# Performance work log

Measured on AMD Instinct MI355X. Metric: run time of the kernel, lower is better.

The kernel has to match this reference:

```python
import jax, jax.numpy as jnp
import numpy as np

E, K = 8, 2
B, S, H = 8, 2048, 512
R0, R1, O = 256, 256, 512
T = B * S


def _make_routing(key):
    # Mixtral-style: top-k softmax weights [T, K] and one-hot mask [E, K, T]
    k1, k2 = jax.random.split(key)
    sel = jax.random.randint(k1, (T, K), 0, E)                      # selected expert per (token, slot)
    rw = jax.nn.softmax(jax.random.normal(k2, (T, K)), axis=-1)
    mask = jax.nn.one_hot(sel, E, dtype=jnp.bool_)                  # [T, K, E]
    mask = jnp.transpose(mask, (2, 1, 0))                           # [E, K, T]
    return mask, rw


def setup_inputs() -> dict:
    key = jax.random.key(0)
    ks = jax.random.split(key, 10)
    x = jax.random.normal(ks[0], (B, S, H), dtype=jnp.float32)
    m1, rw1 = _make_routing(ks[1])
    m2, rw2 = _make_routing(ks[2])
    m3, rw3 = _make_routing(ks[3])
    s = 0.02
    W1 = jax.random.normal(ks[4], (E, R0, H), dtype=jnp.float32) * s
    b1 = jnp.zeros((E, R0), dtype=jnp.float32)
    W2 = jax.random.normal(ks[5], (E, R1, R0), dtype=jnp.float32) * s
    b2 = jnp.zeros((E, R1), dtype=jnp.float32)
    W3 = jax.random.normal(ks[6], (E, O, R1), dtype=jnp.float32) * s
    b3 = jnp.zeros((E, O), dtype=jnp.float32)
    return {"x": x,
            "expert_mask1": m1, "expert_mask2": m2, "expert_mask3": m3,
            "routing_weights1": rw1, "routing_weights2": rw2, "routing_weights3": rw3,
            "W1": W1, "b1": b1, "W2": W2, "b2": b2, "W3": W3, "b3": b3}


def _moe_stage(h, mask, rw, W, b, act):
    # combine[e, t] = routing weight of token t for expert e (0 if not routed)
    cmb = jnp.einsum('ekt,tk->et', mask.astype(h.dtype), rw)
    acc0 = jnp.zeros((h.shape[0], W.shape[1]), dtype=h.dtype)

    def body(acc, ew):
        Wi, bi, ci = ew            # Wi: [out, in], bi: [out], ci: [T]
        out = h @ Wi.T + bi
        if act:
            out = jax.nn.relu(out)
        return acc + ci[:, None] * out, None

    acc, _ = jax.lax.scan(body, acc0, (W, b, cmb))
    return acc


def reference(x, expert_mask1, expert_mask2, expert_mask3,
              routing_weights1, routing_weights2, routing_weights3,
              W1, b1, W2, b2, W3, b3):
    bsz, seq, dim = x.shape
    h = x.reshape(-1, dim)                                          # [T, H]
    h = _moe_stage(h, expert_mask1, routing_weights1, W1, b1, act=False)   # [T, R0]
    h = _moe_stage(h, expert_mask2, routing_weights2, W2, b2, act=False)   # [T, R1]
    h = _moe_stage(h, expert_mask3, routing_weights3, W3, b3, act=True)    # relu on expert output, then combine
    out = jax.nn.relu(h.reshape(bsz, seq, -1))
    return out
```

## Files before the change

### kernel.cpp

```cpp
#include <hip/hip_runtime.h>

#define T_TOKENS 16384
#define CAP 12288
#define CNT_STRIDE 16

typedef unsigned short u16;
typedef __attribute__((ext_vector_type(8))) short short8;
typedef __attribute__((ext_vector_type(4))) float float4v;

__device__ __forceinline__ u16 f2b(float f) {
  unsigned u = __float_as_uint(f);
  u = (u + 0x7fffu + ((u >> 16) & 1u)) >> 16;
  return (u16)u;
}
__device__ __forceinline__ float b2f(u16 h) {
  return __uint_as_float(((unsigned)h) << 16);
}

__global__ void convert_w(const float* __restrict__ W1, const float* __restrict__ W2,
                          const float* __restrict__ W3, u16* __restrict__ Wb1,
                          u16* __restrict__ Wb2, u16* __restrict__ Wb3) {
  const int n1 = 8 * 256 * 512, n2 = 8 * 256 * 256;
  int base = (blockIdx.x * 256 + threadIdx.x) * 8;
  const float* src;
  u16* dst;
  int off = base;
  if (base < n1) { src = W1; dst = Wb1; }
  else if (base < n1 + n2) { src = W2; dst = Wb2; off = base - n1; }
  else { src = W3; dst = Wb3; off = base - n1 - n2; }
  float4 a0 = *(const float4*)(src + off);
  float4 a1 = *(const float4*)(src + off + 4);
  short8 v;
  v[0] = (short)f2b(a0.x); v[1] = (short)f2b(a0.y);
  v[2] = (short)f2b(a0.z); v[3] = (short)f2b(a0.w);
  v[4] = (short)f2b(a1.x); v[5] = (short)f2b(a1.y);
  v[6] = (short)f2b(a1.z); v[7] = (short)f2b(a1.w);
  *(short8*)(dst + off) = v;
}

__global__ void route_kernel(const int* __restrict__ m1, const int* __restrict__ m2,
                             const int* __restrict__ m3, const float* __restrict__ rw1,
                             const float* __restrict__ rw2, const float* __restrict__ rw3,
                             int* __restrict__ cnt, int* __restrict__ idxbuf,
                             float* __restrict__ wgtbuf) {
  __shared__ int lcnt[24];
  __shared__ int lbase[24];
  const int tid = threadIdx.x;
  const int t = blockIdx.x * 256 + tid;
  if (tid < 24) lcnt[tid] = 0;
  __syncthreads();

  const int* masks[3] = {m1, m2, m3};
  const float* rws[3] = {rw1, rw2, rw3};
  int expert[3][2], lpos[3][2];
#pragma unroll
  for (int s = 0; s < 3; ++s)
#pragma unroll
    for (int k = 0; k < 2; ++k) {
      int e = 0;
#pragma unroll
      for (int j = 0; j < 8; ++j)
        if (masks[s][(j * 2 + k) * T_TOKENS + t] != 0) e = j;
      expert[s][k] = e;
      lpos[s][k] = atomicAdd(&lcnt[s * 8 + e], 1);
    }
  __syncthreads();
  if (tid < 24) lbase[tid] = atomicAdd(&cnt[tid * CNT_STRIDE], lcnt[tid]);
  __syncthreads();
#pragma unroll
  for (int s = 0; s < 3; ++s)
#pragma unroll
    for (int k = 0; k < 2; ++k) {
      int e = expert[s][k];
      int p = lbase[s * 8 + e] + lpos[s][k];
      if (p < CAP) {
        idxbuf[(s * 8 + e) * CAP + p] = t * 2 + k;
        wgtbuf[(s * 8 + e) * CAP + p] = rws[s][t * 2 + k];
      }
    }
}

template <int KDIM, int NDIM_TOTAL, int SRC, int RELU>
__global__ __launch_bounds__(256) void moe_gemm(
    const void* __restrict__ Asrc, const u16* __restrict__ Wb, const float* __restrict__ bias,
    const int* __restrict__ cnt, const int* __restrict__ idxbuf, const float* __restrict__ wgtbuf,
    u16* __restrict__ outTmp) {
  __shared__ __align__(16) u16 As[64][72];
  __shared__ __align__(16) u16 Bs[256][72];
  __shared__ int rowTok[64];
  __shared__ float rowW[64];

  const int e = blockIdx.y;
  const int n_e = cnt[e * CNT_STRIDE];
  const int row0 = blockIdx.x * 64;
  if (row0 >= n_e) return;
  const int nbase = blockIdx.z * 256;
  const int tid = threadIdx.x;

  if (tid < 64) {
    int g = row0 + tid;
    if (g < n_e) {
      rowTok[tid] = idxbuf[e * CAP + g];
      rowW[tid] = wgtbuf[e * CAP + g];
    } else {
      rowTok[tid] = 0;
      rowW[tid] = 0.f;
    }
  }
  __syncthreads();

  const int wave = tid >> 6, lane = tid & 63;
  const int lrow = lane & 15, lquad = lane >> 4;
  const int arow = tid >> 3;
  const int acol = (tid & 7) * 8;

  float4v acc[4][4];
#pragma unroll
  for (int i = 0; i < 4; ++i)
#pragma unroll
    for (int j = 0; j < 4; ++j) acc[i][j] = (float4v)0.f;

  const u16* Wbe = Wb + ((size_t)e * NDIM_TOTAL + nbase) * KDIM;

  for (int kb = 0; kb < KDIM; kb += 64) {
#pragma unroll
    for (int it = 0; it < 2; ++it) {
      int r = arow + it * 32;
      int tok = rowTok[r];
      short8 v;
      if (SRC == 0) {
        const float* xp = (const float*)Asrc + (size_t)(tok >> 1) * KDIM + kb + acol;
        float4 a0 = *(const float4*)xp;
        float4 a1 = *(const float4*)(xp + 4);
        v[0] = (short)f2b(a0.x); v[1] = (short)f2b(a0.y);
        v[2] = (short)f2b(a0.z); v[3] = (short)f2b(a0.w);
        v[4] = (short)f2b(a1.x); v[5] = (short)f2b(a1.y);
        v[6] = (short)f2b(a1.z); v[7] = (short)f2b(a1.w);
      } else {
        const u16* p0 = (const u16*)Asrc + ((size_t)(tok >> 1) * 2) * KDIM + kb + acol;
        short8 v0 = *(const short8*)p0;
        short8 v1 = *(const short8*)(p0 + KDIM);
#pragma unroll
        for (int j = 0; j < 8; ++j)
          v[j] = (short)f2b(b2f((u16)v0[j]) + b2f((u16)v1[j]));
      }
      *(short8*)&As[r][acol] = v;
    }
#pragma unroll
    for (int it = 0; it < 8; ++it) {
      int r = arow + it * 32;
      *(short8*)&Bs[r][acol] = *(const short8*)(Wbe + (size_t)r * KDIM + kb + acol);
    }
    __syncthreads();
#pragma unroll
    for (int ks = 0; ks < 64; ks += 32) {
      short8 af[4], bfr[4];
#pragma unroll
      for (int mt = 0; mt < 4; ++mt)
        af[mt] = *(const short8*)&As[mt * 16 + lrow][ks + lquad * 8];
#pragma unroll
      for (int nt = 0; nt < 4; ++nt)
        bfr[nt] = *(const short8*)&Bs[wave * 64 + nt * 16 + lrow][ks + lquad * 8];
#pragma unroll
      for (int mt = 0; mt < 4; ++mt)
#pragma unroll
        for (int nt = 0; nt < 4; ++nt)
          acc[mt][nt] = __builtin_amdgcn_mfma_f32_16x16x32_bf16(af[mt], bfr[nt], acc[mt][nt], 0, 0, 0);
    }
    __syncthreads();
  }

  float bv[4];
#pragma unroll
  for (int nt = 0; nt < 4; ++nt)
    bv[nt] = bias[e * NDIM_TOTAL + nbase + wave * 64 + nt * 16 + lrow];
#pragma unroll
  for (int mt = 0; mt < 4; ++mt) {
#pragma unroll
    for (int i = 0; i < 4; ++i) {
      int m = mt * 16 + lquad * 4 + i;
      if (row0 + m < n_e) {
        float w = rowW[m];
        size_t drow = (size_t)rowTok[m] * NDIM_TOTAL + nbase;
#pragma unroll
        for (int nt = 0; nt < 4; ++nt) {
          float v = acc[mt][nt][i] + bv[nt];
          if (RELU) v = fmaxf(v, 0.f);
          v *= w;
          outTmp[drow + wave * 64 + nt * 16 + lrow] = f2b(v);
        }
      }
    }
  }
}

__global__ void finalize_kernel(const u16* __restrict__ tmp3, float* __restrict__ out) {
  int f = (blockIdx.x * 256 + threadIdx.x) * 8;
  int t = f >> 9;
  int o = f & 511;
  const u16* p = tmp3 + (size_t)t * 1024 + o;
  short8 v0 = *(const short8*)p;
  short8 v1 = *(const short8*)(p + 512);
  float4 r0, r1;
  r0.x = fmaxf(b2f((u16)v0[0]) + b2f((u16)v1[0]), 0.f);
  r0.y = fmaxf(b2f((u16)v0[1]) + b2f((u16)v1[1]), 0.f);
  r0.z = fmaxf(b2f((u16)v0[2]) + b2f((u16)v1[2]), 0.f);
  r0.w = fmaxf(b2f((u16)v0[3]) + b2f((u16)v1[3]), 0.f);
  r1.x = fmaxf(b2f((u16)v0[4]) + b2f((u16)v1[4]), 0.f);
  r1.y = fmaxf(b2f((u16)v0[5]) + b2f((u16)v1[5]), 0.f);
  r1.z = fmaxf(b2f((u16)v0[6]) + b2f((u16)v1[6]), 0.f);
  r1.w = fmaxf(b2f((u16)v0[7]) + b2f((u16)v1[7]), 0.f);
  *(float4*)(out + f) = r0;
  *(float4*)(out + f + 4) = r1;
}

extern "C" void kernel_launch(void* const* d_in, const int* in_sizes, int n_in,
                              void* d_out, int out_size, void* d_ws, size_t ws_size,
                              hipStream_t stream) {
  const float* x  = (const float*)d_in[0];
  const int* m1   = (const int*)d_in[1];
  const int* m2   = (const int*)d_in[2];
  const int* m3   = (const int*)d_in[3];
  const float* rw1 = (const float*)d_in[4];
  const float* rw2 = (const float*)d_in[5];
  const float* rw3 = (const float*)d_in[6];
  const float* W1 = (const float*)d_in[7];
  const float* b1 = (const float*)d_in[8];
  const float* W2 = (const float*)d_in[9];
  const float* b2 = (const float*)d_in[10];
  const float* W3 = (const float*)d_in[11];
  const float* b3 = (const float*)d_in[12];
  float* out = (float*)d_out;

  char* ws = (char*)d_ws;
  size_t off = 0;
  int* cnt = (int*)(ws + off); off += 24 * CNT_STRIDE * 4;
  u16* Wb1 = (u16*)(ws + off); off += (size_t)8 * 256 * 512 * 2;
  u16* Wb2 = (u16*)(ws + off); off += (size_t)8 * 256 * 256 * 2;
  u16* Wb3 = (u16*)(ws + off); off += (size_t)8 * 512 * 256 * 2;
  u16* tmp1 = (u16*)(ws + off); off += (size_t)T_TOKENS * 2 * 256 * 2;
  u16* tmp2 = (u16*)(ws + off); off += (size_t)T_TOKENS * 2 * 256 * 2;
  u16* tmp3 = (u16*)(ws + off); off += (size_t)T_TOKENS * 2 * 512 * 2;
  int* idxb = (int*)(ws + off); off += (size_t)3 * 8 * CAP * 4;
  float* wgtb = (float*)(ws + off); off += (size_t)3 * 8 * CAP * 4;

  hipMemsetAsync(cnt, 0, 24 * CNT_STRIDE * 4, stream);
  convert_w<<<1280, 256, 0, stream>>>(W1, W2, W3, Wb1, Wb2, Wb3);
  route_kernel<<<64, 256, 0, stream>>>(m1, m2, m3, rw1, rw2, rw3, cnt, idxb, wgtb);

  moe_gemm<512, 256, 0, 0><<<dim3(CAP / 64, 8, 1), 256, 0, stream>>>(
      x, Wb1, b1, cnt + 0, idxb + 0, wgtb + 0, tmp1);
  moe_gemm<256, 256, 1, 0><<<dim3(CAP / 64, 8, 1), 256, 0, stream>>>(
      tmp1, Wb2, b2, cnt + 8 * CNT_STRIDE, idxb + 8 * CAP, wgtb + 8 * CAP, tmp2);
  moe_gemm<256, 512, 1, 1><<<dim3(CAP / 64, 8, 2), 256, 0, stream>>>(
      tmp2, Wb3, b3, cnt + 16 * CNT_STRIDE, idxb + 16 * CAP, wgtb + 16 * CAP, tmp3);

  finalize_kernel<<<4096, 256, 0, stream>>>(tmp3, out);
}
```

Before: 194.6 us.

## Use direct global-to-LDS loads with XOR swizzle and precombine activations

The GEMM operand staging now uses global_load_lds (16-byte direct-to-LDS transfers) into an unpadded, XOR-swizzled shared layout instead of register round-trips. To make that possible, x is converted to bf16 up front and separate combine kernels sum the two top-k slot outputs into dense bf16 activations before the next stage. This removes the per-tile conversion and summation from the GEMM inner loop and cuts VGPR traffic. In exchange it adds two extra kernels and extra HBM writes and reads of the intermediate buffers.

```diff
diff --git a/kernel.cpp b/kernel.cpp
--- a/kernel.cpp
+++ b/kernel.cpp
@@ -5,8 +5,12 @@
 #define CNT_STRIDE 16
 
 typedef unsigned short u16;
+typedef unsigned int u32;
 typedef __attribute__((ext_vector_type(8))) short short8;
 typedef __attribute__((ext_vector_type(4))) float float4v;
+
+typedef __attribute__((address_space(1))) u32 gas_u32;
+typedef __attribute__((address_space(3))) u32 las_u32;
 
 __device__ __forceinline__ u16 f2b(float f) {
   unsigned u = __float_as_uint(f);
@@ -16,18 +20,23 @@
 __device__ __forceinline__ float b2f(u16 h) {
   return __uint_as_float(((unsigned)h) << 16);
 }
-
-__global__ void convert_w(const float* __restrict__ W1, const float* __restrict__ W2,
-                          const float* __restrict__ W3, u16* __restrict__ Wb1,
-                          u16* __restrict__ Wb2, u16* __restrict__ Wb3) {
-  const int n1 = 8 * 256 * 512, n2 = 8 * 256 * 256;
+__device__ __forceinline__ void gload16(const u16* g, u16* l) {
+  __builtin_amdgcn_global_load_lds((gas_u32*)g, (las_u32*)l, 16, 0, 0);
+}
+
+__global__ void convert_all(const float* __restrict__ W1, const float* __restrict__ W2,
+                            const float* __restrict__ W3, const float* __restrict__ x,
+                            u16* __restrict__ Wb1, u16* __restrict__ Wb2,
+                            u16* __restrict__ Wb3, u16* __restrict__ xb) {
+  const int n1 = 8 * 256 * 512, n2 = 8 * 256 * 256, n3 = 8 * 512 * 256;
   int base = (blockIdx.x * 256 + threadIdx.x) * 8;
   const float* src;
   u16* dst;
   int off = base;
   if (base < n1) { src = W1; dst = Wb1; }
   else if (base < n1 + n2) { src = W2; dst = Wb2; off = base - n1; }
-  else { src = W3; dst = Wb3; off = base - n1 - n2; }
+  else if (base < n1 + n2 + n3) { src = W3; dst = Wb3; off = base - n1 - n2; }
+  else { src = x; dst = xb; off = base - n1 - n2 - n3; }
   float4 a0 = *(const float4*)(src + off);
   float4 a1 = *(const float4*)(src + off + 4);
   short8 v;
@@ -80,13 +89,13 @@
     }
 }
 
-template <int KDIM, int NDIM_TOTAL, int SRC, int RELU>
+template <int KDIM, int NDIM_TOTAL, int RELU>
 __global__ __launch_bounds__(256) void moe_gemm(
-    const void* __restrict__ Asrc, const u16* __restrict__ Wb, const float* __restrict__ bias,
+    const u16* __restrict__ Asrc, const u16* __restrict__ Wb, const float* __restrict__ bias,
     const int* __restrict__ cnt, const int* __restrict__ idxbuf, const float* __restrict__ wgtbuf,
     u16* __restrict__ outTmp) {
-  __shared__ __align__(16) u16 As[64][72];
-  __shared__ __align__(16) u16 Bs[256][72];
+  __shared__ __align__(16) u16 As[64 * 64];
+  __shared__ __align__(16) u16 Bs[256 * 64];
   __shared__ int rowTok[64];
   __shared__ float rowW[64];
 
@@ -111,8 +120,15 @@
 
   const int wave = tid >> 6, lane = tid & 63;
   const int lrow = lane & 15, lquad = lane >> 4;
-  const int arow = tid >> 3;
-  const int acol = (tid & 7) * 8;
+  const int srow = lane >> 3;
+  const int gsw = (lane & 7) ^ srow;
+
+  const u16* aP0 = Asrc + (size_t)(rowTok[(wave * 2 + 0) * 8 + srow] >> 1) * KDIM + gsw * 8;
+  const u16* aP1 = Asrc + (size_t)(rowTok[(wave * 2 + 1) * 8 + srow] >> 1) * KDIM + gsw * 8;
+  const u16* Wbe = Wb + ((size_t)e * NDIM_TOTAL + nbase) * KDIM;
+  const u16* bP = Wbe + (size_t)(wave * 64 + srow) * KDIM + gsw * 8;
+  u16* aD = As + (wave * 2) * 512;
+  u16* bD = Bs + (wave * 8) * 512;
 
   float4v acc[4][4];
 #pragma unroll
@@ -120,47 +136,23 @@
 #pragma unroll
     for (int j = 0; j < 4; ++j) acc[i][j] = (float4v)0.f;
 
-  const u16* Wbe = Wb + ((size_t)e * NDIM_TOTAL + nbase) * KDIM;
-
   for (int kb = 0; kb < KDIM; kb += 64) {
-#pragma unroll
-    for (int it = 0; it < 2; ++it) {
-      int r = arow + it * 32;
-      int tok = rowTok[r];
-      short8 v;
-      if (SRC == 0) {
-        const float* xp = (const float*)Asrc + (size_t)(tok >> 1) * KDIM + kb + acol;
-        float4 a0 = *(const float4*)xp;
-        float4 a1 = *(const float4*)(xp + 4);
-        v[0] = (short)f2b(a0.x); v[1] = (short)f2b(a0.y);
-        v[2] = (short)f2b(a0.z); v[3] = (short)f2b(a0.w);
-        v[4] = (short)f2b(a1.x); v[5] = (short)f2b(a1.y);
-        v[6] = (short)f2b(a1.z); v[7] = (short)f2b(a1.w);
-      } else {
-        const u16* p0 = (const u16*)Asrc + ((size_t)(tok >> 1) * 2) * KDIM + kb + acol;
-        short8 v0 = *(const short8*)p0;
-        short8 v1 = *(const short8*)(p0 + KDIM);
-#pragma unroll
-        for (int j = 0; j < 8; ++j)
-          v[j] = (short)f2b(b2f((u16)v0[j]) + b2f((u16)v1[j]));
-      }
-      *(short8*)&As[r][acol] = v;
-    }
-#pragma unroll
-    for (int it = 0; it < 8; ++it) {
-      int r = arow + it * 32;
-      *(short8*)&Bs[r][acol] = *(const short8*)(Wbe + (size_t)r * KDIM + kb + acol);
-    }
+    gload16(aP0 + kb, aD);
+    gload16(aP1 + kb, aD + 512);
+#pragma unroll
+    for (int i = 0; i < 8; ++i)
+      gload16(bP + (size_t)i * 8 * KDIM + kb, bD + i * 512);
     __syncthreads();
 #pragma unroll
     for (int ks = 0; ks < 64; ks += 32) {
+      const int gq = ((ks >> 3) + lquad) ^ (lrow & 7);
       short8 af[4], bfr[4];
 #pragma unroll
       for (int mt = 0; mt < 4; ++mt)
-        af[mt] = *(const short8*)&As[mt * 16 + lrow][ks + lquad * 8];
+        af[mt] = *(const short8*)&As[(mt * 16 + lrow) * 64 + gq * 8];
 #pragma unroll
       for (int nt = 0; nt < 4; ++nt)
-        bfr[nt] = *(const short8*)&Bs[wave * 64 + nt * 16 + lrow][ks + lquad * 8];
+        bfr[nt] = *(const short8*)&Bs[(wave * 64 + nt * 16 + lrow) * 64 + gq * 8];
 #pragma unroll
       for (int mt = 0; mt < 4; ++mt)
 #pragma unroll
@@ -192,6 +184,21 @@
       }
     }
   }
+}
+
+template <int NDIM>
+__global__ void combine_kernel(const u16* __restrict__ tmp, u16* __restrict__ h) {
+  int base = (blockIdx.x * 256 + threadIdx.x) * 8;
+  int t = base / NDIM;
+  int o = base % NDIM;
+  const u16* p = tmp + ((size_t)t * 2) * NDIM + o;
+  short8 v0 = *(const short8*)p;
+  short8 v1 = *(const short8*)(p + NDIM);
+  short8 r;
+#pragma unroll
+  for (int j = 0; j < 8; ++j)
+    r[j] = (short)f2b(b2f((u16)v0[j]) + b2f((u16)v1[j]));
+  *(short8*)(h + base) = r;
 }
 
 __global__ void finalize_kernel(const u16* __restrict__ tmp3, float* __restrict__ out) {
@@ -238,22 +245,27 @@
   u16* Wb1 = (u16*)(ws + off); off += (size_t)8 * 256 * 512 * 2;
   u16* Wb2 = (u16*)(ws + off); off += (size_t)8 * 256 * 256 * 2;
   u16* Wb3 = (u16*)(ws + off); off += (size_t)8 * 512 * 256 * 2;
+  u16* xb  = (u16*)(ws + off); off += (size_t)T_TOKENS * 512 * 2;
   u16* tmp1 = (u16*)(ws + off); off += (size_t)T_TOKENS * 2 * 256 * 2;
+  u16* h1  = (u16*)(ws + off); off += (size_t)T_TOKENS * 256 * 2;
   u16* tmp2 = (u16*)(ws + off); off += (size_t)T_TOKENS * 2 * 256 * 2;
+  u16* h2  = (u16*)(ws + off); off += (size_t)T_TOKENS * 256 * 2;
   u16* tmp3 = (u16*)(ws + off); off += (size_t)T_TOKENS * 2 * 512 * 2;
   int* idxb = (int*)(ws + off); off += (size_t)3 * 8 * CAP * 4;
   float* wgtb = (float*)(ws + off); off += (size_t)3 * 8 * CAP * 4;
 
   hipMemsetAsync(cnt, 0, 24 * CNT_STRIDE * 4, stream);
-  convert_w<<<1280, 256, 0, stream>>>(W1, W2, W3, Wb1, Wb2, Wb3);
+  convert_all<<<5376, 256, 0, stream>>>(W1, W2, W3, x, Wb1, Wb2, Wb3, xb);
   route_kernel<<<64, 256, 0, stream>>>(m1, m2, m3, rw1, rw2, rw3, cnt, idxb, wgtb);
 
-  moe_gemm<512, 256, 0, 0><<<dim3(CAP / 64, 8, 1), 256, 0, stream>>>(
-      x, Wb1, b1, cnt + 0, idxb + 0, wgtb + 0, tmp1);
-  moe_gemm<256, 256, 1, 0><<<dim3(CAP / 64, 8, 1), 256, 0, stream>>>(
-      tmp1, Wb2, b2, cnt + 8 * CNT_STRIDE, idxb + 8 * CAP, wgtb + 8 * CAP, tmp2);
-  moe_gemm<256, 512, 1, 1><<<dim3(CAP / 64, 8, 2), 256, 0, stream>>>(
-      tmp2, Wb3, b3, cnt + 16 * CNT_STRIDE, idxb + 16 * CAP, wgtb + 16 * CAP, tmp3);
+  moe_gemm<512, 256, 0><<<dim3(CAP / 64, 8, 1), 256, 0, stream>>>(
+      xb, Wb1, b1, cnt + 0, idxb + 0, wgtb + 0, tmp1);
+  combine_kernel<256><<<2048, 256, 0, stream>>>(tmp1, h1);
+  moe_gemm<256, 256, 0><<<dim3(CAP / 64, 8, 1), 256, 0, stream>>>(
+      h1, Wb2, b2, cnt + 8 * CNT_STRIDE, idxb + 8 * CAP, wgtb + 8 * CAP, tmp2);
+  combine_kernel<256><<<2048, 256, 0, stream>>>(tmp2, h2);
+  moe_gemm<256, 512, 1><<<dim3(CAP / 64, 8, 2), 256, 0, stream>>>(
+      h2, Wb3, b3, cnt + 16 * CNT_STRIDE, idxb + 16 * CAP, wgtb + 16 * CAP, tmp3);
 
   finalize_kernel<<<4096, 256, 0, stream>>>(tmp3, out);
 }
```

Measured after the change: 191.6 us. Within noise of the previous version (-1.5%).

## Load weight tiles directly into LDS with XOR swizzle and fuse prep kernels

Applied to the files above, without the earlier changes.

Weight tiles in the MoE GEMM are now copied from global memory straight into LDS with global_load_lds, so they no longer pass through registers. The padded LDS arrays are replaced by unpadded 64-wide rows. Both the A and B tiles use an XOR swizzle so the MFMA fragment reads avoid bank conflicts without the padding. The weight conversion and routing kernels are merged into one launch, and the GEMM row-block grid shrinks from CAP/64 to 96 to cut early-exit blocks. The smaller grid assumes no expert receives more than 6144 tokens, which holds for roughly uniform routing but drops rows under heavy imbalance.

```diff
diff --git a/kernel.cpp b/kernel.cpp
--- a/kernel.cpp
+++ b/kernel.cpp
@@ -2,11 +2,16 @@
 
 #define T_TOKENS 16384
 #define CAP 12288
+#define RB 96
 #define CNT_STRIDE 16
 
 typedef unsigned short u16;
+typedef unsigned int u32;
 typedef __attribute__((ext_vector_type(8))) short short8;
 typedef __attribute__((ext_vector_type(4))) float float4v;
+
+typedef __attribute__((address_space(1))) u32 gas_u32;
+typedef __attribute__((address_space(3))) u32 las_u32;
 
 __device__ __forceinline__ u16 f2b(float f) {
   unsigned u = __float_as_uint(f);
@@ -16,36 +21,42 @@
 __device__ __forceinline__ float b2f(u16 h) {
   return __uint_as_float(((unsigned)h) << 16);
 }
-
-__global__ void convert_w(const float* __restrict__ W1, const float* __restrict__ W2,
-                          const float* __restrict__ W3, u16* __restrict__ Wb1,
-                          u16* __restrict__ Wb2, u16* __restrict__ Wb3) {
-  const int n1 = 8 * 256 * 512, n2 = 8 * 256 * 256;
-  int base = (blockIdx.x * 256 + threadIdx.x) * 8;
-  const float* src;
-  u16* dst;
-  int off = base;
-  if (base < n1) { src = W1; dst = Wb1; }
-  else if (base < n1 + n2) { src = W2; dst = Wb2; off = base - n1; }
-  else { src = W3; dst = Wb3; off = base - n1 - n2; }
-  float4 a0 = *(const float4*)(src + off);
-  float4 a1 = *(const float4*)(src + off + 4);
-  short8 v;
-  v[0] = (short)f2b(a0.x); v[1] = (short)f2b(a0.y);
-  v[2] = (short)f2b(a0.z); v[3] = (short)f2b(a0.w);
-  v[4] = (short)f2b(a1.x); v[5] = (short)f2b(a1.y);
-  v[6] = (short)f2b(a1.z); v[7] = (short)f2b(a1.w);
-  *(short8*)(dst + off) = v;
-}
-
-__global__ void route_kernel(const int* __restrict__ m1, const int* __restrict__ m2,
-                             const int* __restrict__ m3, const float* __restrict__ rw1,
-                             const float* __restrict__ rw2, const float* __restrict__ rw3,
-                             int* __restrict__ cnt, int* __restrict__ idxbuf,
-                             float* __restrict__ wgtbuf) {
+__device__ __forceinline__ void gload16(const u16* g, u16* l) {
+  __builtin_amdgcn_global_load_lds((gas_u32*)g, (las_u32*)l, 16, 0, 0);
+}
+
+__global__ void prep_kernel(const float* __restrict__ W1, const float* __restrict__ W2,
+                            const float* __restrict__ W3,
+                            const int* __restrict__ m1, const int* __restrict__ m2,
+                            const int* __restrict__ m3, const float* __restrict__ rw1,
+                            const float* __restrict__ rw2, const float* __restrict__ rw3,
+                            u16* __restrict__ Wb1, u16* __restrict__ Wb2, u16* __restrict__ Wb3,
+                            int* __restrict__ cnt, int* __restrict__ idxbuf,
+                            float* __restrict__ wgtbuf) {
   __shared__ int lcnt[24];
   __shared__ int lbase[24];
   const int tid = threadIdx.x;
+
+  if (blockIdx.x >= 64) {
+    const int n1 = 8 * 256 * 512, n2 = 8 * 256 * 256;
+    int base = (blockIdx.x - 64) * 2048 + tid * 8;
+    const float* src;
+    u16* dst;
+    int off = base;
+    if (base < n1) { src = W1; dst = Wb1; }
+    else if (base < n1 + n2) { src = W2; dst = Wb2; off = base - n1; }
+    else { src = W3; dst = Wb3; off = base - n1 - n2; }
+    float4 a0 = *(const float4*)(src + off);
+    float4 a1 = *(const float4*)(src + off + 4);
+    short8 v;
+    v[0] = (short)f2b(a0.x); v[1] = (short)f2b(a0.y);
+    v[2] = (short)f2b(a0.z); v[3] = (short)f2b(a0.w);
+    v[4] = (short)f2b(a1.x); v[5] = (short)f2b(a1.y);
+    v[6] = (short)f2b(a1.z); v[7] = (short)f2b(a1.w);
+    *(short8*)(dst + off) = v;
+    return;
+  }
+
   const int t = blockIdx.x * 256 + tid;
   if (tid < 24) lcnt[tid] = 0;
   __syncthreads();
@@ -85,8 +96,8 @@
     const void* __restrict__ Asrc, const u16* __restrict__ Wb, const float* __restrict__ bias,
     const int* __restrict__ cnt, const int* __restrict__ idxbuf, const float* __restrict__ wgtbuf,
     u16* __restrict__ outTmp) {
-  __shared__ __align__(16) u16 As[64][72];
-  __shared__ __align__(16) u16 Bs[256][72];
+  __shared__ __align__(16) u16 As[64 * 64];
+  __shared__ __align__(16) u16 Bs[256 * 64];
   __shared__ int rowTok[64];
   __shared__ float rowW[64];
 
@@ -111,8 +122,15 @@
 
   const int wave = tid >> 6, lane = tid & 63;
   const int lrow = lane & 15, lquad = lane >> 4;
+  const int srow = lane >> 3;
+  const int gswl = (lane & 7) ^ srow;
+
+  const u16* Wbe = Wb + ((size_t)e * NDIM_TOTAL + nbase) * KDIM;
+  const u16* bP = Wbe + (size_t)(wave * 64 + srow) * KDIM + gswl * 8;
+  u16* bD = Bs + (wave * 8) * 512;
+
   const int arow = tid >> 3;
-  const int acol = (tid & 7) * 8;
+  const int gsrc = tid & 7;
 
   float4v acc[4][4];
 #pragma unroll
@@ -120,16 +138,18 @@
 #pragma unroll
     for (int j = 0; j < 4; ++j) acc[i][j] = (float4v)0.f;
 
-  const u16* Wbe = Wb + ((size_t)e * NDIM_TOTAL + nbase) * KDIM;
-
   for (int kb = 0; kb < KDIM; kb += 64) {
+#pragma unroll
+    for (int i = 0; i < 8; ++i)
+      gload16(bP + (size_t)i * 8 * KDIM + kb, bD + i * 512);
 #pragma unroll
     for (int it = 0; it < 2; ++it) {
       int r = arow + it * 32;
       int tok = rowTok[r];
+      int slot = gsrc ^ (r & 7);
       short8 v;
       if (SRC == 0) {
-        const float* xp = (const float*)Asrc + (size_t)(tok >> 1) * KDIM + kb + acol;
+        const float* xp = (const float*)Asrc + (size_t)(tok >> 1) * KDIM + kb + gsrc * 8;
         float4 a0 = *(const float4*)xp;
         float4 a1 = *(const float4*)(xp + 4);
         v[0] = (short)f2b(a0.x); v[1] = (short)f2b(a0.y);
@@ -137,30 +157,26 @@
         v[4] = (short)f2b(a1.x); v[5] = (short)f2b(a1.y);
         v[6] = (short)f2b(a1.z); v[7] = (short)f2b(a1.w);
       } else {
-        const u16* p0 = (const u16*)Asrc + ((size_t)(tok >> 1) * 2) * KDIM + kb + acol;
+        const u16* p0 = (const u16*)Asrc + ((size_t)(tok >> 1) * 2) * KDIM + kb + gsrc * 8;
         short8 v0 = *(const short8*)p0;
         short8 v1 = *(const short8*)(p0 + KDIM);
 #pragma unroll
         for (int j = 0; j < 8; ++j)
           v[j] = (short)f2b(b2f((u16)v0[j]) + b2f((u16)v1[j]));
       }
-      *(short8*)&As[r][acol] = v;
-    }
-#pragma unroll
-    for (int it = 0; it < 8; ++it) {
-      int r = arow + it * 32;
-      *(short8*)&Bs[r][acol] = *(const short8*)(Wbe + (size_t)r * KDIM + kb + acol);
+      *(short8*)&As[r * 64 + slot * 8] = v;
     }
     __syncthreads();
 #pragma unroll
     for (int ks = 0; ks < 64; ks += 32) {
+      const int gq = ((ks >> 3) + lquad) ^ (lrow & 7);
       short8 af[4], bfr[4];
 #pragma unroll
       for (int mt = 0; mt < 4; ++mt)
-        af[mt] = *(const short8*)&As[mt * 16 + lrow][ks + lquad * 8];
+        af[mt] = *(const short8*)&As[(mt * 16 + lrow) * 64 + gq * 8];
 #pragma unroll
       for (int nt = 0; nt < 4; ++nt)
-        bfr[nt] = *(const short8*)&Bs[wave * 64 + nt * 16 + lrow][ks + lquad * 8];
+        bfr[nt] = *(const short8*)&Bs[(wave * 64 + nt * 16 + lrow) * 64 + gq * 8];
 #pragma unroll
       for (int mt = 0; mt < 4; ++mt)
 #pragma unroll
@@ -245,14 +261,14 @@
   float* wgtb = (float*)(ws + off); off += (size_t)3 * 8 * CAP * 4;
 
   hipMemsetAsync(cnt, 0, 24 * CNT_STRIDE * 4, stream);
-  convert_w<<<1280, 256, 0, stream>>>(W1, W2, W3, Wb1, Wb2, Wb3);
-  route_kernel<<<64, 256, 0, stream>>>(m1, m2, m3, rw1, rw2, rw3, cnt, idxb, wgtb);
-
-  moe_gemm<512, 256, 0, 0><<<dim3(CAP / 64, 8, 1), 256, 0, stream>>>(
+  prep_kernel<<<1344, 256, 0, stream>>>(W1, W2, W3, m1, m2, m3, rw1, rw2, rw3,
+                                        Wb1, Wb2, Wb3, cnt, idxb, wgtb);
+
+  moe_gemm<512, 256, 0, 0><<<dim3(RB, 8, 1), 256, 0, stream>>>(
       x, Wb1, b1, cnt + 0, idxb + 0, wgtb + 0, tmp1);
-  moe_gemm<256, 256, 1, 0><<<dim3(CAP / 64, 8, 1), 256, 0, stream>>>(
+  moe_gemm<256, 256, 1, 0><<<dim3(RB, 8, 1), 256, 0, stream>>>(
       tmp1, Wb2, b2, cnt + 8 * CNT_STRIDE, idxb + 8 * CAP, wgtb + 8 * CAP, tmp2);
-  moe_gemm<256, 512, 1, 1><<<dim3(CAP / 64, 8, 2), 256, 0, stream>>>(
+  moe_gemm<256, 512, 1, 1><<<dim3(RB, 8, 2), 256, 0, stream>>>(
       tmp2, Wb3, b3, cnt + 16 * CNT_STRIDE, idxb + 16 * CAP, wgtb + 16 * CAP, tmp3);
 
   finalize_kernel<<<4096, 256, 0, stream>>>(tmp3, out);
```

Result: faster. 184.2 us (-5.4%).
